# Kernel tuning notes

Hardware: AMD Instinct MI355X
Metric: run time of the kernel (lower is better)

The kernel has to match this reference:

```python
import jax, jax.numpy as jnp
import numpy as np

B, S, D, H, DM, SS, A, HID = 2048, 64, 6, 4, 64, 150, 7, 256
FF = 4 * DM
DH = DM // H

def layernorm(x, g, b, eps=1e-5):
    m = jnp.mean(x, axis=-1, keepdims=True)
    v = jnp.mean((x - m) ** 2, axis=-1, keepdims=True)
    return (x - m) * jax.lax.rsqrt(v + eps) * g + b

def setup_inputs() -> dict:
    key = jax.random.key(0)
    ks = jax.random.split(key, 24)
    w = lambda k, sh: jax.random.normal(k, sh, dtype=jnp.float32) * 0.05
    inp = {
        'observation': jax.random.normal(ks[0], (B, SS), dtype=jnp.float32),
        'sequence': jax.random.normal(ks[1], (S, B, SS), dtype=jnp.float32),
        'memory': jax.random.normal(ks[2], (D, B, S, DM), dtype=jnp.float32) * 0.1,
        'length': jax.random.randint(ks[3], (1, B, 1), 0, S, dtype=jnp.int32),
        # input LayerNorm (state_size=150)
        'ln_g': jnp.ones((SS,), jnp.float32), 'ln_b': jnp.zeros((SS,), jnp.float32),
        # token_embedding replaced by Identity in source; embedding_dim(150)->dim(64) projection
        'W_emb': w(ks[4], (SS, DM)),
        # per-layer transformer params (stacked over depth)
        'ln1_g': jnp.ones((D, DM), jnp.float32), 'ln1_b': jnp.zeros((D, DM), jnp.float32),
        'ln2_g': jnp.ones((D, DM), jnp.float32), 'ln2_b': jnp.zeros((D, DM), jnp.float32),
        'Wq': w(ks[5], (D, DM, DM)), 'Wk': w(ks[6], (D, DM, DM)),
        'Wv': w(ks[7], (D, DM, DM)), 'Wo': w(ks[8], (D, DM, DM)),
        'W1': w(ks[9], (D, DM, FF)), 'b1': jnp.zeros((D, FF), jnp.float32),
        'W2': w(ks[10], (D, FF, DM)), 'b2': jnp.zeros((D, DM), jnp.float32),
        # policy MLP: dim -> 256 -> 2*action_size
        'Wp1': w(ks[11], (DM, HID)), 'bp1': jnp.zeros((HID,), jnp.float32),
        'Wp2': w(ks[12], (HID, 2 * A)), 'bp2': jnp.zeros((2 * A,), jnp.float32),
    }
    return inp

def reference(observation, sequence, memory, ln_g, ln_b, W_emb,
              ln1_g, ln1_b, ln2_g, ln2_b, Wq, Wk, Wv, Wo, W1, b1, W2, b2,
              Wp1, bp1, Wp2, bp2, length):
    # sample_forward (T == 1)
    obs = layernorm(observation, ln_g, ln_b)                      # (B,150)
    lidx = jnp.clip(length[0, :, 0], 0, S - 1)                    # (B,)
    bidx = jnp.arange(B)
    # index_put_: scatter current obs into sequence buffer at per-batch position
    seq = sequence.at[lidx, bidx].set(obs)                        # (S,B,150)
    x = jnp.einsum('bse,ed->bsd', seq.transpose(1, 0, 2), W_emb)  # (B,S,DM)
    # queries attend fully to the memory segment, causally within current segment
    causal = jnp.tril(jnp.ones((S, S), bool))
    mask = jnp.concatenate([jnp.ones((S, S), bool), causal], axis=1)  # (S, 2S)
    scale = 1.0 / np.sqrt(DH)
    new_mems = []
    for l in range(D):
        new_mems.append(x)                                        # hidden entering layer -> new memory
        h = layernorm(x, ln1_g[l], ln1_b[l])
        kv_in = jnp.concatenate([memory[l], h], axis=1)           # (B,2S,DM)
        q = (h @ Wq[l]).reshape(B, S, H, DH)
        k = (kv_in @ Wk[l]).reshape(B, 2 * S, H, DH)
        v = (kv_in @ Wv[l]).reshape(B, 2 * S, H, DH)
        scores = jnp.einsum('bqhd,bkhd->bhqk', q, k) * scale      # (B,H,S,2S)
        scores = jnp.where(mask[None, None], scores, jnp.finfo(scores.dtype).min)
        attn = jax.nn.softmax(scores, axis=-1)
        out = jnp.einsum('bhqk,bkhd->bqhd', attn, v).reshape(B, S, DM)
        x = x + out @ Wo[l]
        h2 = layernorm(x, ln2_g[l], ln2_b[l])
        x = x + jax.nn.relu(h2 @ W1[l] + b1[l]) @ W2[l] + b2[l]
    new_memory = jnp.stack(new_mems)                              # (D,B,S,DM)
    out_sb = x.transpose(1, 0, 2)                                 # (S,B,DM)
    output = out_sb[lidx, bidx]                                   # gather by length -> (B,DM)
    new_length = jnp.mod(length + 1, S)                           # (1,B,1)
    reset = (new_length[0, :, 0] == 0).astype(memory.dtype)[None, :, None, None]
    mem_out = reset * new_memory + (1.0 - reset) * memory         # masked memory reset/blend
    # policy head
    pol = jax.nn.relu(output @ Wp1 + bp1) @ Wp2 + bp2             # (B, 2A)
    std = jax.nn.softplus(pol[:, :A])
    mu = jnp.tanh(pol[:, A:])
    return (mu, std, seq, mem_out, new_length)
```

## Files before the change

### kernel.cpp

```cpp
#include <hip/hip_runtime.h>
#include <hip/hip_bf16.h>
#include <math.h>

#define NB 2048

#define LD4(p) (*(const float4*)(p))

#define O_STD 14336
#define O_SEQ 28672
#define O_MEM 19689472
#define O_LEN 70021120

#define WQT 0
#define WKT 24576
#define WVT 49152
#define WOT 73728
#define W1T 98304
#define W2T 196608
#define WET 294912

typedef __attribute__((ext_vector_type(8))) short short8v;
typedef __attribute__((ext_vector_type(4))) float f32x4;

#define MFMA(a, b, c) __builtin_amdgcn_mfma_f32_16x16x32_bf16((a), (b), (c), 0, 0, 0)

#define QSC 0.36067376022224087f

#define R_SKV   0
#define R_A1    8192
#define R_VT    12288
#define R_WO    20480
#define R_H2    24576
#define R_W2B0  28672
#define R_W2B1  32768

__device__ __forceinline__ short f2bf(float f) {
    return __builtin_bit_cast(short, (__bf16)f);
}
__device__ __forceinline__ unsigned pk2(float lo, float hi) {
    union { __hip_bfloat162 h; unsigned u; } t;
    t.h = __float22bfloat162_rn(make_float2(lo, hi));
    return t.u;
}

__global__ __launch_bounds__(256) void prep_weights(
        const float* __restrict__ Wq, const float* __restrict__ Wk,
        const float* __restrict__ Wv, const float* __restrict__ Wo,
        const float* __restrict__ W1, const float* __restrict__ W2,
        const float* __restrict__ Wemb, short* __restrict__ wsb) {
    int idx = blockIdx.x * 256 + threadIdx.x;
    {
        int l = idx >> 14, r = idx & 16383;
        { int n = r >> 6, k = r & 63;
          wsb[W1T + idx] = f2bf(W1[l * 16384 + k * 256 + n]); }
        { int n = r >> 8, k = r & 255;
          wsb[W2T + idx] = f2bf(W2[l * 16384 + k * 64 + n]); }
    }
    if (idx < 24576) {
        int l = idx >> 12, r = idx & 4095;
        int n = r >> 6, k = r & 63;
        int s = l * 4096 + k * 64 + n;
        wsb[WQT + idx] = f2bf(Wq[s]);
        wsb[WKT + idx] = f2bf(Wk[s]);
        wsb[WVT + idx] = f2bf(Wv[s]);
        wsb[WOT + idx] = f2bf(Wo[s]);
    }
    if (idx < 10240) {
        int n = idx / 160, k = idx - n * 160;
        wsb[WET + idx] = (k < 150) ? f2bf(Wemb[k * 64 + n]) : (short)0;
    }
}

__global__ __launch_bounds__(256) void copy4_kernel(const float4* __restrict__ src,
                                                    float4* __restrict__ dst, int n) {
    int i = blockIdx.x * 256 + threadIdx.x;
    if (i < n) dst[i] = src[i];
}

__global__ __launch_bounds__(256) void obs_ln_kernel(const float* __restrict__ obs,
        const float* __restrict__ g, const float* __restrict__ be,
        const int* __restrict__ len, float* __restrict__ outSeq, float* __restrict__ outLen) {
    int w = threadIdx.x >> 6, lane = threadIdx.x & 63;
    int b = blockIdx.x * 4 + w;
    const float* row = obs + (size_t)b * 150;
    float v0 = row[lane], v1 = row[64 + lane];
    float v2 = (lane < 22) ? row[128 + lane] : 0.f;
    float s = v0 + v1 + v2;
    #pragma unroll
    for (int m = 1; m <= 32; m <<= 1) s += __shfl_xor(s, m);
    float mean = s * (1.0f / 150.0f);
    float d0 = v0 - mean, d1 = v1 - mean;
    float d2 = (lane < 22) ? (v2 - mean) : 0.f;
    float q = d0 * d0 + d1 * d1 + d2 * d2;
    #pragma unroll
    for (int m = 1; m <= 32; m <<= 1) q += __shfl_xor(q, m);
    float rs = rsqrtf(q * (1.0f / 150.0f) + 1e-5f);
    int lenraw = len[b];
    int lidx = min(max(lenraw, 0), 63);
    float* orow = outSeq + ((size_t)lidx * NB + b) * 150;
    orow[lane]      = d0 * rs * g[lane] + be[lane];
    orow[64 + lane] = d1 * rs * g[64 + lane] + be[64 + lane];
    if (lane < 22) orow[128 + lane] = d2 * rs * g[128 + lane] + be[128 + lane];
    if (lane == 0) outLen[b] = (float)((lenraw + 1) & 63);
}

__global__ __launch_bounds__(256, 2) void mega_kernel(
        const float* __restrict__ seq, const float* __restrict__ memory,
        const int* __restrict__ len,
        const float* __restrict__ ln1g, const float* __restrict__ ln1b,
        const float* __restrict__ ln2g, const float* __restrict__ ln2b,
        const float* __restrict__ b1, const float* __restrict__ b2,
        const short* __restrict__ wsb,
        float* __restrict__ memOut, float* __restrict__ xrow) {
    __shared__ short L[36864];
    __shared__ float fls[576];
    float* lnp = fls;
    float* b1f = fls + 256;
    float* b2f = fls + 512;

    const int tid = threadIdx.x;
    const int b = blockIdx.x;
    const int w = tid >> 6;
    const int lane = tid & 63;
    const int g = lane >> 4;
    const int r16 = lane & 15;

    const int lenraw = len[b];
    const int lidx = min(max(lenraw, 0), 63);
    const bool reset = (((lenraw + 1) & 63) == 0);

    const int cxa = (r16 & 7) << 3;
    const int fc0 = (8 * g) ^ cxa;
    const int fc1 = (32 + 8 * g) ^ cxa;
    const int cxw = (g & 1) << 5;
    const int cxm = ((tid >> 2) & 7) << 3;

    const short8v zs = {0, 0, 0, 0, 0, 0, 0, 0};
    const f32x4 zf = {0.f, 0.f, 0.f, 0.f};

    #pragma unroll 1
    for (int j = 0; j < 16; ++j) {
        int r = w * 16 + j;
        int rb = r * 160;
        const float* srow = seq + ((size_t)r * NB + b) * 150;
        L[rb + lane]      = f2bf(srow[lane]);
        L[rb + 64 + lane] = f2bf(srow[64 + lane]);
        if (lane < 22)      L[rb + 128 + lane] = f2bf(srow[128 + lane]);
        else if (lane < 32) L[rb + 128 + lane] = 0;
    }
    {
        const int4* s4p = (const int4*)(wsb + WET);
        int4* d4p = (int4*)(L + 10240);
        #pragma unroll
        for (int i = 0; i < 5; ++i) d4p[tid + i * 256] = s4p[tid + i * 256];
    }
    __syncthreads();

    f32x4 x[4] = {zf, zf, zf, zf};
    #pragma unroll
    for (int kk = 0; kk < 5; ++kk) {
        short8v a = *(const short8v*)&L[(16 * w + r16) * 160 + kk * 32 + 8 * g];
        #pragma unroll
        for (int ct = 0; ct < 4; ++ct) {
            short8v bb = *(const short8v*)&L[10240 + (16 * ct + r16) * 160 + kk * 32 + 8 * g];
            x[ct] = MFMA(a, bb, x[ct]);
        }
    }
    __syncthreads();

    #pragma unroll 1
    for (int l = 0; l < 6; ++l) {
        auto stage_sq = [&](const short* src, int dstbase) {
            const int4* s = (const int4*)src;
            int4* d = (int4*)(L + dstbase);
            #pragma unroll
            for (int i = 0; i < 2; ++i) {
                int idx = tid + i * 256;
                d[idx ^ ((idx >> 3) & 7)] = s[idx];
            }
        };
        auto stage_w2 = [&](int kb, int dstbase) {
            int4* d = (int4*)(L + dstbase);
            #pragma unroll
            for (int i = 0; i < 2; ++i) {
                int idx = tid + i * 256;
                int sx = idx ^ ((idx >> 3) & 7);
                int n = idx >> 3, c = idx & 7;
                d[sx] = *(const int4*)&wsb[W2T + l * 16384 + n * 256 + kb * 64 + c * 8];
            }
        };

        if (tid < 64) {
            lnp[tid]       = ln1g[l * 64 + tid];
            lnp[64 + tid]  = ln1b[l * 64 + tid];
            lnp[128 + tid] = ln2g[l * 64 + tid];
            lnp[192 + tid] = ln2b[l * 64 + tid];
            b2f[tid]       = b2[l * 64 + tid];
        }
        b1f[tid] = b1[l * 256 + tid];
        {
            const float* gmem = memory + ((size_t)l * NB + b) * 4096;
            float* gout = memOut + ((size_t)l * NB + b) * 4096;
            int rr = tid >> 2, c0 = (tid & 3) * 16;
            #pragma unroll
            for (int k4 = 0; k4 < 4; ++k4) {
                float4 v = LD4(&gmem[rr * 64 + c0 + k4 * 4]);
                if (!reset) *(float4*)&gout[rr * 64 + c0 + k4 * 4] = v;
                uint2 su;
                su.x = pk2(v.x, v.y); su.y = pk2(v.z, v.w);
                *(uint2*)&L[rr * 64 + ((c0 + k4 * 4) ^ cxm)] = su;
            }
            if (reset) {
                #pragma unroll
                for (int ct = 0; ct < 4; ++ct)
                    #pragma unroll
                    for (int j = 0; j < 4; ++j)
                        gout[(16 * w + 4 * g + j) * 64 + 16 * ct + r16] = x[ct][j];
            }
        }
        stage_sq(wsb + WQT + l * 4096, R_A1);
        stage_sq(wsb + WKT + l * 4096, R_VT);
        stage_sq(wsb + WVT + l * 4096, R_VT + 4096);
        stage_sq(wsb + WOT + l * 4096, R_WO);
        stage_w2(0, R_W2B0);
        stage_w2(1, R_W2B1);
        __syncthreads();

        #pragma unroll
        for (int j = 0; j < 4; ++j) {
            float s = x[0][j] + x[1][j] + x[2][j] + x[3][j];
            s += __shfl_xor(s, 1); s += __shfl_xor(s, 2);
            s += __shfl_xor(s, 4); s += __shfl_xor(s, 8);
            float m = s * 0.015625f;
            float q = 0.f;
            #pragma unroll
            for (int ct = 0; ct < 4; ++ct) { float d = x[ct][j] - m; q += d * d; }
            q += __shfl_xor(q, 1); q += __shfl_xor(q, 2);
            q += __shfl_xor(q, 4); q += __shfl_xor(q, 8);
            float rs = rsqrtf(q * 0.015625f + 1e-5f);
            #pragma unroll
            for (int ct = 0; ct < 4; ++ct) {
                int col = 16 * ct + r16;
                float hv = (x[ct][j] - m) * rs * lnp[col] + lnp[64 + col];
                L[(64 + 16 * w + 4 * g + j) * 64 + (col ^ (cxw | (j << 3)))] = f2bf(hv);
            }
        }

        f32x4 qa[4] = {zf, zf, zf, zf};
        f32x4 ka[2][4] = {{zf, zf, zf, zf}, {zf, zf, zf, zf}};
        #pragma unroll
        for (int kk = 0; kk < 2; ++kk) {
            const int fc = kk ? fc1 : fc0;
            short8v ah = *(const short8v*)&L[(64 + 16 * w + r16) * 64 + fc];
            short8v a0 = *(const short8v*)&L[(16 * w + r16) * 64 + fc];
            #pragma unroll
            for (int ct = 0; ct < 4; ++ct) {
                short8v bq = *(const short8v*)&L[R_A1 + (16 * ct + r16) * 64 + fc];
                short8v bk = *(const short8v*)&L[R_VT + (16 * ct + r16) * 64 + fc];
                qa[ct]    = MFMA(ah, bq, qa[ct]);
                ka[0][ct] = MFMA(a0, bk, ka[0][ct]);
                ka[1][ct] = MFMA(ah, bk, ka[1][ct]);
            }
        }
        #pragma unroll
        for (int ct = 0; ct < 4; ++ct)
            #pragma unroll
            for (int j = 0; j < 4; ++j)
                L[R_H2 + (16 * w + 4 * g + j) * 64 + ((16 * ct + r16) ^ (cxw | (j << 3)))] =
                    f2bf(qa[ct][j] * QSC);

        f32x4 va[2][4] = {{zf, zf, zf, zf}, {zf, zf, zf, zf}};
        #pragma unroll
        for (int kk = 0; kk < 2; ++kk) {
            const int fc = kk ? fc1 : fc0;
            short8v ah = *(const short8v*)&L[(64 + 16 * w + r16) * 64 + fc];
            short8v a0 = *(const short8v*)&L[(16 * w + r16) * 64 + fc];
            #pragma unroll
            for (int ct = 0; ct < 4; ++ct) {
                short8v bv = *(const short8v*)&L[R_VT + 4096 + (16 * ct + r16) * 64 + fc];
                va[0][ct] = MFMA(a0, bv, va[0][ct]);
                va[1][ct] = MFMA(ah, bv, va[1][ct]);
            }
        }
        __syncthreads();

        #pragma unroll
        for (int ct = 0; ct < 4; ++ct) {
            #pragma unroll
            for (int j = 0; j < 4; ++j) {
                int key0 = 16 * w + 4 * g + j;
                int colw = (16 * ct + r16) ^ (cxw | (j << 3));
                L[key0 * 64 + colw] = f2bf(ka[0][ct][j]);
                L[(64 + key0) * 64 + colw] = f2bf(ka[1][ct][j]);
            }
        }
        {
            const int p0 = ((w >> 1) << 5) | (g << 3) | ((w & 1) << 2);
            const int p1 = p0 | 64;
            #pragma unroll
            for (int ct = 0; ct < 4; ++ct) {
                int rowb = R_VT + (16 * ct + r16) * 128;
                uint2 v0, v1;
                v0.x = pk2(va[0][ct][0], va[0][ct][1]);
                v0.y = pk2(va[0][ct][2], va[0][ct][3]);
                v1.x = pk2(va[1][ct][0], va[1][ct][1]);
                v1.y = pk2(va[1][ct][2], va[1][ct][3]);
                *(uint2*)&L[rowb + (p0 ^ cxa)] = v0;
                *(uint2*)&L[rowb + (p1 ^ cxa)] = v1;
            }
        }
        __syncthreads();

        const int hc = 16 * w;
        const int attc = (hc + 8 * g) ^ cxa;
        const int obc  = (hc + 4 * g) ^ cxa;
        #pragma unroll
        for (int qt = 0; qt < 4; ++qt) {
            const int KT = 5 + qt;
            short8v bQ = (g < 2) ? *(const short8v*)&L[R_H2 + (16 * qt + r16) * 64 + attc] : zs;
            f32x4 s[8];
            #pragma unroll
            for (int kt = 0; kt < 8; ++kt) if (kt < KT) {
                short8v aK = *(const short8v*)&L[(16 * kt + r16) * 64 + attc];
                s[kt] = MFMA(aK, bQ, zf);
            }
            float sum = 0.f;
            #pragma unroll
            for (int kt = 0; kt < 8; ++kt) if (kt < KT) {
                #pragma unroll
                for (int j = 0; j < 4; ++j) {
                    float e = exp2f(s[kt][j]);
                    if (kt == KT - 1) e = ((4 * g + j) > r16) ? 0.f : e;
                    s[kt][j] = e; sum += e;
                }
            }
            sum += __shfl_xor(sum, 16);
            sum += __shfl_xor(sum, 32);
            float inv = 1.0f / sum;
            f32x4 of = zf;
            const int KT2 = (KT + 1) >> 1;
            #pragma unroll
            for (int kt2 = 0; kt2 < 4; ++kt2) if (kt2 < KT2) {
                short8v aV = *(const short8v*)&L[R_VT + (hc + r16) * 128 +
                                                 ((32 * kt2 + 8 * g) ^ cxa)];
                union { short8v v; unsigned u[4]; } pb;
                const int i0 = 2 * kt2, i1 = 2 * kt2 + 1;
                pb.u[0] = pk2(s[i0][0], s[i0][1]);
                pb.u[1] = pk2(s[i0][2], s[i0][3]);
                pb.u[2] = (i1 < KT) ? pk2(s[i1][0], s[i1][1]) : 0u;
                pb.u[3] = (i1 < KT) ? pk2(s[i1][2], s[i1][3]) : 0u;
                of = MFMA(aV, pb.v, of);
            }
            uint2 ov;
            ov.x = pk2(of[0] * inv, of[1] * inv);
            ov.y = pk2(of[2] * inv, of[3] * inv);
            *(uint2*)&L[R_A1 + (16 * qt + r16) * 64 + obc] = ov;
        }
        __syncthreads();

        stage_sq(wsb + W1T + l * 16384, R_SKV);
        stage_sq(wsb + W1T + l * 16384 + 4096, R_SKV + 4096);

        #pragma unroll
        for (int kk = 0; kk < 2; ++kk) {
            const int fc = kk ? fc1 : fc0;
            short8v a = *(const short8v*)&L[R_A1 + (16 * w + r16) * 64 + fc];
            #pragma unroll
            for (int ct = 0; ct < 4; ++ct) {
                short8v bb = *(const short8v*)&L[R_WO + (16 * ct + r16) * 64 + fc];
                x[ct] = MFMA(a, bb, x[ct]);
            }
        }
        #pragma unroll
        for (int j = 0; j < 4; ++j) {
            float s = x[0][j] + x[1][j] + x[2][j] + x[3][j];
            s += __shfl_xor(s, 1); s += __shfl_xor(s, 2);
            s += __shfl_xor(s, 4); s += __shfl_xor(s, 8);
            float m = s * 0.015625f;
            float q = 0.f;
            #pragma unroll
            for (int ct = 0; ct < 4; ++ct) { float d = x[ct][j] - m; q += d * d; }
            q += __shfl_xor(q, 1); q += __shfl_xor(q, 2);
            q += __shfl_xor(q, 4); q += __shfl_xor(q, 8);
            float rs = rsqrtf(q * 0.015625f + 1e-5f);
            #pragma unroll
            for (int ct = 0; ct < 4; ++ct) {
                int col = 16 * ct + r16;
                float hv = (x[ct][j] - m) * rs * lnp[128 + col] + lnp[192 + col];
                L[R_H2 + (16 * w + 4 * g + j) * 64 + (col ^ (cxw | (j << 3)))] = f2bf(hv);
            }
        }

        auto ff_step = [&](int w1b, int w2b, int kb) {
            f32x4 tacc[4] = {zf, zf, zf, zf};
            #pragma unroll
            for (int kk = 0; kk < 2; ++kk) {
                const int fc = kk ? fc1 : fc0;
                short8v a = *(const short8v*)&L[R_H2 + (16 * w + r16) * 64 + fc];
                #pragma unroll
                for (int ct = 0; ct < 4; ++ct) {
                    short8v bb = *(const short8v*)&L[w1b + (16 * ct + r16) * 64 + fc];
                    tacc[ct] = MFMA(a, bb, tacc[ct]);
                }
            }
            #pragma unroll
            for (int ct = 0; ct < 4; ++ct)
                #pragma unroll
                for (int j = 0; j < 4; ++j) {
                    float v = fmaxf(tacc[ct][j] + b1f[kb * 64 + 16 * ct + r16], 0.f);
                    L[R_A1 + (16 * w + 4 * g + j) * 64 + ((16 * ct + r16) ^ (cxw | (j << 3)))] = f2bf(v);
                }
            #pragma unroll
            for (int kk = 0; kk < 2; ++kk) {
                const int fc = kk ? fc1 : fc0;
                short8v a = *(const short8v*)&L[R_A1 + (16 * w + r16) * 64 + fc];
                #pragma unroll
                for (int ct = 0; ct < 4; ++ct) {
                    short8v bb = *(const short8v*)&L[w2b + (16 * ct + r16) * 64 + fc];
                    x[ct] = MFMA(a, bb, x[ct]);
                }
            }
        };

        __syncthreads();
        ff_step(R_SKV, R_W2B0, 0);
        __syncthreads();
        stage_sq(wsb + W1T + l * 16384 + 2 * 4096, R_SKV);
        stage_w2(2, R_W2B0);
        ff_step(R_SKV + 4096, R_W2B1, 1);
        __syncthreads();
        stage_sq(wsb + W1T + l * 16384 + 3 * 4096, R_SKV + 4096);
        stage_w2(3, R_W2B1);
        ff_step(R_SKV, R_W2B0, 2);
        __syncthreads();
        ff_step(R_SKV + 4096, R_W2B1, 3);
        #pragma unroll
        for (int ct = 0; ct < 4; ++ct)
            #pragma unroll
            for (int j = 0; j < 4; ++j) x[ct][j] += b2f[16 * ct + r16];
        __syncthreads();
    }

    if (w == (lidx >> 4) && g == ((lidx >> 2) & 3)) {
        int j = lidx & 3;
        #pragma unroll
        for (int ct = 0; ct < 4; ++ct) {
            float v = (j == 0) ? x[ct][0] : (j == 1) ? x[ct][1] : (j == 2) ? x[ct][2] : x[ct][3];
            xrow[(size_t)b * 64 + 16 * ct + r16] = v;
        }
    }
}

__device__ __forceinline__ float softplusf(float v) {
    return fmaxf(v, 0.f) + log1pf(expf(-fabsf(v)));
}

__global__ __launch_bounds__(256) void policy_kernel(const float* __restrict__ xrow,
        const float* __restrict__ Wp1, const float* __restrict__ bp1,
        const float* __restrict__ Wp2, const float* __restrict__ bp2,
        float* __restrict__ outMu, float* __restrict__ outStd) {
    __shared__ float sx[64];
    __shared__ float sh1[256];
    const int tid = threadIdx.x;
    for (int bi = 0; bi < 16; ++bi) {
        int b = blockIdx.x * 16 + bi;
        if (tid < 64) sx[tid] = xrow[(size_t)b * 64 + tid];
        __syncthreads();
        float acc = bp1[tid];
        #pragma unroll 16
        for (int k = 0; k < 64; ++k) acc = fmaf(sx[k], Wp1[k * 256 + tid], acc);
        sh1[tid] = fmaxf(acc, 0.f);
        __syncthreads();
        if (tid < 224) {
            int j = tid >> 4, gg = tid & 15;
            float a = 0.f;
            #pragma unroll
            for (int kk = 0; kk < 16; ++kk) {
                int k = gg * 16 + kk;
                a = fmaf(sh1[k], Wp2[k * 14 + j], a);
            }
            a += __shfl_xor(a, 1); a += __shfl_xor(a, 2);
            a += __shfl_xor(a, 4); a += __shfl_xor(a, 8);
            if (gg == 0) {
                float pol = a + bp2[j];
                if (j < 7) outStd[(size_t)b * 7 + j] = softplusf(pol);
                else       outMu[(size_t)b * 7 + (j - 7)] = tanhf(pol);
            }
        }
        __syncthreads();
    }
}

extern "C" void kernel_launch(void* const* d_in, const int* in_sizes, int n_in,
                              void* d_out, int out_size, void* d_ws, size_t ws_size,
                              hipStream_t stream) {
    const float* obs   = (const float*)d_in[0];
    const float* seqIn = (const float*)d_in[1];
    const float* mem   = (const float*)d_in[2];
    const int*   len   = (const int*)d_in[3];
    const float* ln_g  = (const float*)d_in[4];
    const float* ln_b  = (const float*)d_in[5];
    const float* Wemb  = (const float*)d_in[6];
    const float* ln1g  = (const float*)d_in[7];
    const float* ln1b  = (const float*)d_in[8];
    const float* ln2g  = (const float*)d_in[9];
    const float* ln2b  = (const float*)d_in[10];
    const float* Wq    = (const float*)d_in[11];
    const float* Wk    = (const float*)d_in[12];
    const float* Wv    = (const float*)d_in[13];
    const float* Wo    = (const float*)d_in[14];
    const float* W1    = (const float*)d_in[15];
    const float* b1    = (const float*)d_in[16];
    const float* W2    = (const float*)d_in[17];
    const float* b2    = (const float*)d_in[18];
    const float* Wp1   = (const float*)d_in[19];
    const float* bp1   = (const float*)d_in[20];
    const float* Wp2   = (const float*)d_in[21];
    const float* bp2   = (const float*)d_in[22];

    float* out    = (float*)d_out;
    float* outMu  = out;
    float* outStd = out + O_STD;
    float* outSeq = out + O_SEQ;
    float* outMem = out + O_MEM;
    float* outLen = out + O_LEN;
    float* xrow   = (float*)d_ws;
    short* wsb    = (short*)((char*)d_ws + 524288);

    hipLaunchKernelGGL(prep_weights, dim3(384), dim3(256), 0, stream,
                       Wq, Wk, Wv, Wo, W1, W2, Wemb, wsb);
    hipLaunchKernelGGL(copy4_kernel, dim3(19200), dim3(256), 0, stream,
                       (const float4*)seqIn, (float4*)outSeq, 4915200);
    hipLaunchKernelGGL(obs_ln_kernel, dim3(512), dim3(256), 0, stream,
                       obs, ln_g, ln_b, len, outSeq, outLen);
    hipLaunchKernelGGL(mega_kernel, dim3(2048), dim3(256), 0, stream,
                       outSeq, mem, len, ln1g, ln1b, ln2g, ln2b, b1, b2,
                       wsb, outMem, xrow);
    hipLaunchKernelGGL(policy_kernel, dim3(128), dim3(256), 0, stream,
                       xrow, Wp1, bp1, Wp2, bp2, outMu, outStd);
}
```

Baseline: 493.3 us.

## Read transformer weights directly from global memory instead of staging in LDS

```diff
diff --git a/kernel.cpp b/kernel.cpp
--- a/kernel.cpp
+++ b/kernel.cpp
@@ -29,10 +29,7 @@
 #define R_SKV   0
 #define R_A1    8192
 #define R_VT    12288
-#define R_WO    20480
-#define R_H2    24576
-#define R_W2B0  28672
-#define R_W2B1  32768
+#define R_H2    20480
 
 __device__ __forceinline__ short f2bf(float f) {
     return __builtin_bit_cast(short, (__bf16)f);
@@ -104,7 +101,7 @@
     if (lane == 0) outLen[b] = (float)((lenraw + 1) & 63);
 }
 
-__global__ __launch_bounds__(256, 2) void mega_kernel(
+__global__ __launch_bounds__(256, 3) void mega_kernel(
         const float* __restrict__ seq, const float* __restrict__ memory,
         const int* __restrict__ len,
         const float* __restrict__ ln1g, const float* __restrict__ ln1b,
@@ -112,7 +109,7 @@
         const float* __restrict__ b1, const float* __restrict__ b2,
         const short* __restrict__ wsb,
         float* __restrict__ memOut, float* __restrict__ xrow) {
-    __shared__ short L[36864];
+    __shared__ short L[24576];
     __shared__ float fls[576];
     float* lnp = fls;
     float* b1f = fls + 256;
@@ -132,6 +129,8 @@
     const int cxa = (r16 & 7) << 3;
     const int fc0 = (8 * g) ^ cxa;
     const int fc1 = (32 + 8 * g) ^ cxa;
+    const int gc0 = 8 * g;
+    const int gc1 = 32 + 8 * g;
     const int cxw = (g & 1) << 5;
     const int cxm = ((tid >> 2) & 7) << 3;
 
@@ -170,25 +169,12 @@
 
     #pragma unroll 1
     for (int l = 0; l < 6; ++l) {
-        auto stage_sq = [&](const short* src, int dstbase) {
-            const int4* s = (const int4*)src;
-            int4* d = (int4*)(L + dstbase);
-            #pragma unroll
-            for (int i = 0; i < 2; ++i) {
-                int idx = tid + i * 256;
-                d[idx ^ ((idx >> 3) & 7)] = s[idx];
-            }
-        };
-        auto stage_w2 = [&](int kb, int dstbase) {
-            int4* d = (int4*)(L + dstbase);
-            #pragma unroll
-            for (int i = 0; i < 2; ++i) {
-                int idx = tid + i * 256;
-                int sx = idx ^ ((idx >> 3) & 7);
-                int n = idx >> 3, c = idx & 7;
-                d[sx] = *(const int4*)&wsb[W2T + l * 16384 + n * 256 + kb * 64 + c * 8];
-            }
-        };
+        const short* wqg = wsb + WQT + l * 4096;
+        const short* wkg = wsb + WKT + l * 4096;
+        const short* wvg = wsb + WVT + l * 4096;
+        const short* wog = wsb + WOT + l * 4096;
+        const short* w1g = wsb + W1T + l * 16384;
+        const short* w2g = wsb + W2T + l * 16384;
 
         if (tid < 64) {
             lnp[tid]       = ln1g[l * 64 + tid];
@@ -218,12 +204,6 @@
                         gout[(16 * w + 4 * g + j) * 64 + 16 * ct + r16] = x[ct][j];
             }
         }
-        stage_sq(wsb + WQT + l * 4096, R_A1);
-        stage_sq(wsb + WKT + l * 4096, R_VT);
-        stage_sq(wsb + WVT + l * 4096, R_VT + 4096);
-        stage_sq(wsb + WOT + l * 4096, R_WO);
-        stage_w2(0, R_W2B0);
-        stage_w2(1, R_W2B1);
         __syncthreads();
 
         #pragma unroll
@@ -251,12 +231,14 @@
         #pragma unroll
         for (int kk = 0; kk < 2; ++kk) {
             const int fc = kk ? fc1 : fc0;
+            const int gcol = kk ? gc1 : gc0;
             short8v ah = *(const short8v*)&L[(64 + 16 * w + r16) * 64 + fc];
             short8v a0 = *(const short8v*)&L[(16 * w + r16) * 64 + fc];
             #pragma unroll
             for (int ct = 0; ct < 4; ++ct) {
-                short8v bq = *(const short8v*)&L[R_A1 + (16 * ct + r16) * 64 + fc];
-                short8v bk = *(const short8v*)&L[R_VT + (16 * ct + r16) * 64 + fc];
+                const int ro = (16 * ct + r16) * 64 + gcol;
+                short8v bq = *(const short8v*)&wqg[ro];
+                short8v bk = *(const short8v*)&wkg[ro];
                 qa[ct]    = MFMA(ah, bq, qa[ct]);
                 ka[0][ct] = MFMA(a0, bk, ka[0][ct]);
                 ka[1][ct] = MFMA(ah, bk, ka[1][ct]);
@@ -273,16 +255,16 @@
         #pragma unroll
         for (int kk = 0; kk < 2; ++kk) {
             const int fc = kk ? fc1 : fc0;
+            const int gcol = kk ? gc1 : gc0;
             short8v ah = *(const short8v*)&L[(64 + 16 * w + r16) * 64 + fc];
             short8v a0 = *(const short8v*)&L[(16 * w + r16) * 64 + fc];
             #pragma unroll
             for (int ct = 0; ct < 4; ++ct) {
-                short8v bv = *(const short8v*)&L[R_VT + 4096 + (16 * ct + r16) * 64 + fc];
+                short8v bv = *(const short8v*)&wvg[(16 * ct + r16) * 64 + gcol];
                 va[0][ct] = MFMA(a0, bv, va[0][ct]);
                 va[1][ct] = MFMA(ah, bv, va[1][ct]);
             }
         }
-        __syncthreads();
 
         #pragma unroll
         for (int ct = 0; ct < 4; ++ct) {
@@ -358,16 +340,14 @@
         }
         __syncthreads();
 
-        stage_sq(wsb + W1T + l * 16384, R_SKV);
-        stage_sq(wsb + W1T + l * 16384 + 4096, R_SKV + 4096);
-
         #pragma unroll
         for (int kk = 0; kk < 2; ++kk) {
             const int fc = kk ? fc1 : fc0;
+            const int gcol = kk ? gc1 : gc0;
             short8v a = *(const short8v*)&L[R_A1 + (16 * w + r16) * 64 + fc];
             #pragma unroll
             for (int ct = 0; ct < 4; ++ct) {
-                short8v bb = *(const short8v*)&L[R_WO + (16 * ct + r16) * 64 + fc];
+                short8v bb = *(const short8v*)&wog[(16 * ct + r16) * 64 + gcol];
                 x[ct] = MFMA(a, bb, x[ct]);
             }
         }
@@ -391,15 +371,17 @@
             }
         }
 
-        auto ff_step = [&](int w1b, int w2b, int kb) {
+        #pragma unroll
+        for (int kb = 0; kb < 4; ++kb) {
             f32x4 tacc[4] = {zf, zf, zf, zf};
             #pragma unroll
             for (int kk = 0; kk < 2; ++kk) {
                 const int fc = kk ? fc1 : fc0;
+                const int gcol = kk ? gc1 : gc0;
                 short8v a = *(const short8v*)&L[R_H2 + (16 * w + r16) * 64 + fc];
                 #pragma unroll
                 for (int ct = 0; ct < 4; ++ct) {
-                    short8v bb = *(const short8v*)&L[w1b + (16 * ct + r16) * 64 + fc];
+                    short8v bb = *(const short8v*)&w1g[(kb * 64 + 16 * ct + r16) * 64 + gcol];
                     tacc[ct] = MFMA(a, bb, tacc[ct]);
                 }
             }
@@ -413,27 +395,15 @@
             #pragma unroll
             for (int kk = 0; kk < 2; ++kk) {
                 const int fc = kk ? fc1 : fc0;
+                const int gcol = kk ? gc1 : gc0;
                 short8v a = *(const short8v*)&L[R_A1 + (16 * w + r16) * 64 + fc];
                 #pragma unroll
                 for (int ct = 0; ct < 4; ++ct) {
-                    short8v bb = *(const short8v*)&L[w2b + (16 * ct + r16) * 64 + fc];
+                    short8v bb = *(const short8v*)&w2g[(16 * ct + r16) * 256 + kb * 64 + gcol];
                     x[ct] = MFMA(a, bb, x[ct]);
                 }
             }
-        };
-
-        __syncthreads();
-        ff_step(R_SKV, R_W2B0, 0);
-        __syncthreads();
-        stage_sq(wsb + W1T + l * 16384 + 2 * 4096, R_SKV);
-        stage_w2(2, R_W2B0);
-        ff_step(R_SKV + 4096, R_W2B1, 1);
-        __syncthreads();
-        stage_sq(wsb + W1T + l * 16384 + 3 * 4096, R_SKV + 4096);
-        stage_w2(3, R_W2B1);
-        ff_step(R_SKV, R_W2B0, 2);
-        __syncthreads();
-        ff_step(R_SKV + 4096, R_W2B1, 3);
+        }
         #pragma unroll
         for (int ct = 0; ct < 4; ++ct)
             #pragma unroll
```

Result: slower. 1.013 ms (+105.4%).

## Fuse sequence copy and policy head into mega kernel

Applied to the files above, without the earlier changes.

```diff
diff --git a/kernel.cpp b/kernel.cpp
--- a/kernel.cpp
+++ b/kernel.cpp
@@ -41,6 +41,10 @@
     union { __hip_bfloat162 h; unsigned u; } t;
     t.h = __float22bfloat162_rn(make_float2(lo, hi));
     return t.u;
+}
+
+__device__ __forceinline__ float softplusf(float v) {
+    return fmaxf(v, 0.f) + log1pf(expf(-fabsf(v)));
 }
 
 __global__ __launch_bounds__(256) void prep_weights(
@@ -69,12 +73,6 @@
         int n = idx / 160, k = idx - n * 160;
         wsb[WET + idx] = (k < 150) ? f2bf(Wemb[k * 64 + n]) : (short)0;
     }
-}
-
-__global__ __launch_bounds__(256) void copy4_kernel(const float4* __restrict__ src,
-                                                    float4* __restrict__ dst, int n) {
-    int i = blockIdx.x * 256 + threadIdx.x;
-    if (i < n) dst[i] = src[i];
 }
 
 __global__ __launch_bounds__(256) void obs_ln_kernel(const float* __restrict__ obs,
@@ -105,13 +103,18 @@
 }
 
 __global__ __launch_bounds__(256, 2) void mega_kernel(
-        const float* __restrict__ seq, const float* __restrict__ memory,
+        const float* __restrict__ seqIn,
+        float* __restrict__ outSeq,
+        const float* __restrict__ memory,
         const int* __restrict__ len,
         const float* __restrict__ ln1g, const float* __restrict__ ln1b,
         const float* __restrict__ ln2g, const float* __restrict__ ln2b,
         const float* __restrict__ b1, const float* __restrict__ b2,
         const short* __restrict__ wsb,
-        float* __restrict__ memOut, float* __restrict__ xrow) {
+        const float* __restrict__ Wp1, const float* __restrict__ bp1,
+        const float* __restrict__ Wp2, const float* __restrict__ bp2,
+        float* __restrict__ memOut,
+        float* __restrict__ outMu, float* __restrict__ outStd) {
     __shared__ short L[36864];
     __shared__ float fls[576];
     float* lnp = fls;
@@ -142,11 +145,20 @@
     for (int j = 0; j < 16; ++j) {
         int r = w * 16 + j;
         int rb = r * 160;
-        const float* srow = seq + ((size_t)r * NB + b) * 150;
-        L[rb + lane]      = f2bf(srow[lane]);
-        L[rb + 64 + lane] = f2bf(srow[64 + lane]);
-        if (lane < 22)      L[rb + 128 + lane] = f2bf(srow[128 + lane]);
-        else if (lane < 32) L[rb + 128 + lane] = 0;
+        const size_t ro = ((size_t)r * NB + b) * 150;
+        const float* srow = (r == lidx) ? (outSeq + ro) : (seqIn + ro);
+        float v0 = srow[lane];
+        float v1 = srow[64 + lane];
+        float v2 = (lane < 22) ? srow[128 + lane] : 0.f;
+        if (r != lidx) {
+            float* orow = outSeq + ro;
+            orow[lane]      = v0;
+            orow[64 + lane] = v1;
+            if (lane < 22) orow[128 + lane] = v2;
+        }
+        L[rb + lane]      = f2bf(v0);
+        L[rb + 64 + lane] = f2bf(v1);
+        if (lane < 32) L[rb + 128 + lane] = (lane < 22) ? f2bf(v2) : (short)0;
     }
     {
         const int4* s4p = (const int4*)(wsb + WET);
@@ -446,48 +458,32 @@
         #pragma unroll
         for (int ct = 0; ct < 4; ++ct) {
             float v = (j == 0) ? x[ct][0] : (j == 1) ? x[ct][1] : (j == 2) ? x[ct][2] : x[ct][3];
-            xrow[(size_t)b * 64 + 16 * ct + r16] = v;
-        }
-    }
-}
-
-__device__ __forceinline__ float softplusf(float v) {
-    return fmaxf(v, 0.f) + log1pf(expf(-fabsf(v)));
-}
-
-__global__ __launch_bounds__(256) void policy_kernel(const float* __restrict__ xrow,
-        const float* __restrict__ Wp1, const float* __restrict__ bp1,
-        const float* __restrict__ Wp2, const float* __restrict__ bp2,
-        float* __restrict__ outMu, float* __restrict__ outStd) {
-    __shared__ float sx[64];
-    __shared__ float sh1[256];
-    const int tid = threadIdx.x;
-    for (int bi = 0; bi < 16; ++bi) {
-        int b = blockIdx.x * 16 + bi;
-        if (tid < 64) sx[tid] = xrow[(size_t)b * 64 + tid];
-        __syncthreads();
+            lnp[16 * ct + r16] = v;
+        }
+    }
+    __syncthreads();
+    {
         float acc = bp1[tid];
         #pragma unroll 16
-        for (int k = 0; k < 64; ++k) acc = fmaf(sx[k], Wp1[k * 256 + tid], acc);
-        sh1[tid] = fmaxf(acc, 0.f);
-        __syncthreads();
-        if (tid < 224) {
-            int j = tid >> 4, gg = tid & 15;
-            float a = 0.f;
-            #pragma unroll
-            for (int kk = 0; kk < 16; ++kk) {
-                int k = gg * 16 + kk;
-                a = fmaf(sh1[k], Wp2[k * 14 + j], a);
-            }
-            a += __shfl_xor(a, 1); a += __shfl_xor(a, 2);
-            a += __shfl_xor(a, 4); a += __shfl_xor(a, 8);
-            if (gg == 0) {
-                float pol = a + bp2[j];
-                if (j < 7) outStd[(size_t)b * 7 + j] = softplusf(pol);
-                else       outMu[(size_t)b * 7 + (j - 7)] = tanhf(pol);
-            }
-        }
-        __syncthreads();
+        for (int k = 0; k < 64; ++k) acc = fmaf(lnp[k], Wp1[k * 256 + tid], acc);
+        b1f[tid] = fmaxf(acc, 0.f);
+    }
+    __syncthreads();
+    if (tid < 224) {
+        int j = tid >> 4, gg = tid & 15;
+        float a = 0.f;
+        #pragma unroll
+        for (int kk = 0; kk < 16; ++kk) {
+            int k = gg * 16 + kk;
+            a = fmaf(b1f[k], Wp2[k * 14 + j], a);
+        }
+        a += __shfl_xor(a, 1); a += __shfl_xor(a, 2);
+        a += __shfl_xor(a, 4); a += __shfl_xor(a, 8);
+        if (gg == 0) {
+            float pol = a + bp2[j];
+            if (j < 7) outStd[(size_t)b * 7 + j] = softplusf(pol);
+            else       outMu[(size_t)b * 7 + (j - 7)] = tanhf(pol);
+        }
     }
 }
 
@@ -524,18 +520,13 @@
     float* outSeq = out + O_SEQ;
     float* outMem = out + O_MEM;
     float* outLen = out + O_LEN;
-    float* xrow   = (float*)d_ws;
     short* wsb    = (short*)((char*)d_ws + 524288);
 
     hipLaunchKernelGGL(prep_weights, dim3(384), dim3(256), 0, stream,
                        Wq, Wk, Wv, Wo, W1, W2, Wemb, wsb);
-    hipLaunchKernelGGL(copy4_kernel, dim3(19200), dim3(256), 0, stream,
-                       (const float4*)seqIn, (float4*)outSeq, 4915200);
     hipLaunchKernelGGL(obs_ln_kernel, dim3(512), dim3(256), 0, stream,
                        obs, ln_g, ln_b, len, outSeq, outLen);
     hipLaunchKernelGGL(mega_kernel, dim3(2048), dim3(256), 0, stream,
-                       outSeq, mem, len, ln1g, ln1b, ln2g, ln2b, b1, b2,
-                       wsb, outMem, xrow);
-    hipLaunchKernelGGL(policy_kernel, dim3(128), dim3(256), 0, stream,
-                       xrow, Wp1, bp1, Wp2, bp2, outMu, outStd);
-}
+                       seqIn, outSeq, mem, len, ln1g, ln1b, ln2g, ln2b, b1, b2,
+                       wsb, Wp1, bp1, Wp2, bp2, outMem, outMu, outStd);
+}
```

After: 441.4 us. 1.12x faster.
